# Optimization experiments

Hardware: AMD Instinct MI355X
Metric: run time of the kernel (lower is better)

The kernel has to match this reference:

```python
import jax, jax.numpy as jnp
import numpy as np

N_NODES = 100000
DIM = 256
N_SAMPLES = 64
N_CLASSES = 10


def setup_inputs() -> dict:
    key = jax.random.key(0)
    k1, k2, k3 = jax.random.split(key, 3)
    data = jax.random.normal(k1, (N_SAMPLES, DIM), dtype=jnp.float32)
    V = jax.random.uniform(k2, (N_NODES, DIM), dtype=jnp.float32)  # node matrix (torch.rand init)
    labels = jax.random.randint(k3, (N_SAMPLES,), 0, N_CLASSES)
    return {"data": data, "V": V, "labels": labels, "it": 0}


def reference(data, V, labels, it):
    # SOINN+ per-sample BMU search + BMU/sBMU weight pull, fixed node capacity.
    # eps schedules exactly as in ASOINN.forward.
    eps_b = 1.0 / (it + 2)
    eps_n = 1.0 / ((it + 1) * 100)

    def step(Vc, sample):
        # pairwise L2 distance of sample vs all nodes: [N]
        diff = sample[None, :] - Vc
        dists = jnp.sqrt(jnp.sum(diff * diff, axis=-1) + 1e-12)
        neg_vals, idx = jax.lax.top_k(-dists, 2)  # two smallest
        b, s = idx[0], idx[1]
        # update_bmu: V[b] += eps_b * (sample - V[b]); neighbor pull on sBMU
        Vc = Vc.at[b].add(eps_b * (sample - Vc[b]))
        Vc = Vc.at[s].add(eps_n * (sample - Vc[s]))
        return Vc, -neg_vals  # (b_dist, s_dist)

    V_final, bmu_dists = jax.lax.scan(step, V, data)
    return bmu_dists  # [N_SAMPLES, 2]
```

## Files before the change

kernel.cpp:

```cpp
#include <hip/hip_runtime.h>
#include <math.h>


#define N_NODES 100000
#define DIM     256
#define NS      64
#define NCH     1563
#define KC      32
#define NBMW    3125
#define CAP     4096
#define KL      192
#define KLS     136
#define NSP     10
#define NPW     8

typedef unsigned long long u64;

__device__ __forceinline__ u64 pk(float d, int i) {
  return ((u64)__float_as_uint(d) << 32) | (unsigned)i;
}
__device__ __forceinline__ u64 umin64(u64 a, u64 b) { return a < b ? a : b; }
__device__ __forceinline__ u64 umax64(u64 a, u64 b) { return a > b ? a : b; }
__device__ __forceinline__ void mrg2(u64& A0, u64& A1, u64 B0, u64 B1) {
  u64 m = umax64(A0, B0);
  A0 = umin64(A0, B0);
  A1 = umin64(umin64(A1, B1), m);
}

template <int C>
__device__ __forceinline__ u64 dpp64(u64 x) {
  unsigned lo = (unsigned)__builtin_amdgcn_update_dpp(
      (int)0xFFFFFFFF, (int)(unsigned)(x & 0xFFFFFFFFull), C, 0xF, 0xF, false);
  unsigned hi = (unsigned)__builtin_amdgcn_update_dpp(
      (int)0xFFFFFFFF, (int)(unsigned)(x >> 32), C, 0xF, 0xF, false);
  return ((u64)hi << 32) | lo;
}
template <int C>
__device__ __forceinline__ void dpp_round(u64& A0, u64& A1) {
  u64 B0 = dpp64<C>(A0);
  u64 B1 = dpp64<C>(A1);
  mrg2(A0, A1, B0, B1);
}

__global__ void k_xx(const float* __restrict__ X, float* __restrict__ XX) {
  int i = blockIdx.x, j = threadIdx.x;
  const float* xi = X + i * DIM;
  const float* xj = X + j * DIM;
  float acc = 0.f;
  for (int k = 0; k < DIM; k += 4) {
    float4 a = *(const float4*)(xi + k);
    float4 b = *(const float4*)(xj + k);
    acc += a.x * b.x + a.y * b.y + a.z * b.z + a.w * b.w;
  }
  XX[i * NS + j] = acc;
}

__global__ __launch_bounds__(256) void k_dist(const float* __restrict__ X,
                                              const float* __restrict__ V,
                                              const float* __restrict__ XX,
                                              float* __restrict__ P,
                                              float* __restrict__ PT,
                                              float* __restrict__ Q,
                                              u64* __restrict__ SUMC) {
  __shared__ float Xl[KC][68];
  __shared__ float Vl[KC][132];
  __shared__ float sq[128];
  const int tid = threadIdx.x;
  const int n0  = blockIdx.x * 128;
  const int ty  = tid >> 5;
  const int tx  = tid & 31;
  float acc[8][4];
#pragma unroll
  for (int i = 0; i < 8; i++)
#pragma unroll
    for (int u = 0; u < 4; u++) acc[i][u] = 0.f;
  float qa = 0.f;
  const int xsl = tid & 63;
  const int xkk = (tid >> 6) * 8;
  const int vn  = tid & 127;
  const int vkk = (tid >> 7) * 16;
  const bool vok = (n0 + vn < N_NODES);
  const float* vrow = V + (size_t)(n0 + vn) * DIM + vkk;
  const float* xrow = X + xsl * DIM + xkk;

  float4 xr0, xr1, vr[4];
  xr0 = *(const float4*)(xrow + 0);
  xr1 = *(const float4*)(xrow + 4);
#pragma unroll
  for (int m = 0; m < 4; m++)
    vr[m] = vok ? *(const float4*)(vrow + 4 * m) : make_float4(0.f, 0.f, 0.f, 0.f);

  for (int c = 0; c < 8; c++) {
    __syncthreads();
    Xl[xkk + 0][xsl] = xr0.x; Xl[xkk + 1][xsl] = xr0.y;
    Xl[xkk + 2][xsl] = xr0.z; Xl[xkk + 3][xsl] = xr0.w;
    Xl[xkk + 4][xsl] = xr1.x; Xl[xkk + 5][xsl] = xr1.y;
    Xl[xkk + 6][xsl] = xr1.z; Xl[xkk + 7][xsl] = xr1.w;
#pragma unroll
    for (int m = 0; m < 4; m++) {
      Vl[vkk + 4 * m + 0][vn] = vr[m].x; Vl[vkk + 4 * m + 1][vn] = vr[m].y;
      Vl[vkk + 4 * m + 2][vn] = vr[m].z; Vl[vkk + 4 * m + 3][vn] = vr[m].w;
    }
    __syncthreads();
    if (c + 1 < 8) {
      int kc = (c + 1) * KC;
      xr0 = *(const float4*)(xrow + kc);
      xr1 = *(const float4*)(xrow + kc + 4);
#pragma unroll
      for (int m = 0; m < 4; m++)
        vr[m] = vok ? *(const float4*)(vrow + kc + 4 * m)
                    : make_float4(0.f, 0.f, 0.f, 0.f);
    }
    if (tid < 128) {
      float qq = 0.f;
#pragma unroll 8
      for (int k = 0; k < KC; k++) { float t = Vl[k][tid]; qq += t * t; }
      qa += qq;
    }
#pragma unroll 4
    for (int k = 0; k < KC; k++) {
      float xs[8], vs[4];
      *(float4*)&xs[0] = *(const float4*)&Xl[k][ty * 8];
      *(float4*)&xs[4] = *(const float4*)&Xl[k][ty * 8 + 4];
      *(float4*)&vs[0] = *(const float4*)&Vl[k][tx * 4];
#pragma unroll
      for (int i = 0; i < 8; i++)
#pragma unroll
        for (int u = 0; u < 4; u++) acc[i][u] += xs[i] * vs[u];
    }
  }
  if (tid < 128) sq[tid] = qa;
  __syncthreads();
  if (tid < 128 && n0 + tid < N_NODES) Q[n0 + tid] = qa;
  float qs[4];
  *(float4*)&qs[0] = *(const float4*)&sq[tx * 4];
  const bool full = (n0 + 128) <= N_NODES;
#pragma unroll
  for (int i = 0; i < 8; i++) {
    int s = ty * 8 + i;
    float xn = XX[s * NS + s];
#pragma unroll
    for (int u = 0; u < 4; u++) acc[i][u] = xn - 2.f * acc[i][u] + qs[u];
    float* prow = P + (size_t)s * N_NODES + n0 + tx * 4;
    if (full) {
      *(float4*)(prow) = make_float4(acc[i][0], acc[i][1], acc[i][2], acc[i][3]);
    } else {
#pragma unroll
      for (int u = 0; u < 4; u++) {
        int n = n0 + tx * 4 + u;
        if (n < N_NODES) prow[u] = acc[i][u];
      }
    }
  }
#pragma unroll
  for (int u = 0; u < 4; u++) {
    int n = n0 + tx * 4 + u;
    if (n < N_NODES) {
      float* pt = PT + (size_t)n * NS + ty * 8;
      *(float4*)(pt)     = make_float4(acc[0][u], acc[1][u], acc[2][u], acc[3][u]);
      *(float4*)(pt + 4) = make_float4(acc[4][u], acc[5][u], acc[6][u], acc[7][u]);
    }
  }
#pragma unroll
  for (int i = 0; i < 8; i++) {
    int s = ty * 8 + i;
    u64 key = ~0ull;
#pragma unroll
    for (int u = 0; u < 4; u++) {
      int n = n0 + tx * 4 + u;
      if (n < N_NODES) key = umin64(key, pk(acc[i][u], n));
    }
#pragma unroll
    for (int off = 1; off <= 8; off <<= 1)
      key = umin64(key, (u64)__shfl_xor((unsigned long long)key, off, 64));
    if ((tx & 15) == 0) {
      int chunk = (n0 >> 6) + (tx >> 4);
      if (chunk < NCH) SUMC[(size_t)s * NCH + chunk] = key;
    }
  }
}

__global__ __launch_bounds__(1024) void k_build(const u64* __restrict__ SUMC,
                                                const float* __restrict__ P,
                                                u64* __restrict__ L) {
  __shared__ u64 A[CAP];
  __shared__ u64 Twave[16];
  __shared__ float Tsh;
  __shared__ int cnt;
  const int j = blockIdx.x, tid = threadIdx.x;
  const int w = tid >> 6, l = tid & 63;
  {
    int base = w * 98;
    u64 v0 = (base + l < NCH) ? SUMC[(size_t)j * NCH + base + l] : ~0ull;
    u64 v1 = (l < 34 && base + 64 + l < NCH)
                 ? SUMC[(size_t)j * NCH + base + 64 + l] : ~0ull;
    u64 s9 = ~0ull;
#pragma unroll
    for (int r = 0; r < 9; r++) {
      u64 m = umin64(v0, v1);
#pragma unroll
      for (int off = 1; off <= 32; off <<= 1)
        m = umin64(m, (u64)__shfl_xor((unsigned long long)m, off, 64));
      if (r == 8) { s9 = m; } else {
        if (v0 == m) v0 = ~0ull;
        if (v1 == m) v1 = ~0ull;
      }
    }
    if (l == 0) Twave[w] = s9;
  }
  __syncthreads();
  if (tid == 0) {
    u64 t = 0;
    for (int i = 0; i < 16; i++) t = umax64(t, Twave[i]);
    Tsh = __uint_as_float((unsigned)(t >> 32));
    cnt = 0;
  }
  __syncthreads();
  const float T = Tsh;
  const float* prow = P + (size_t)j * N_NODES;
  for (int n0 = tid * 4; n0 < N_NODES + 3; n0 += 4096) {
    float d[4];
    if (n0 + 3 < N_NODES) {
      float4 p = *(const float4*)(prow + n0);
      d[0] = p.x; d[1] = p.y; d[2] = p.z; d[3] = p.w;
    } else {
#pragma unroll
      for (int e = 0; e < 4; e++)
        d[e] = (n0 + e < N_NODES) ? prow[n0 + e] : INFINITY;
    }
#pragma unroll
    for (int e = 0; e < 4; e++) {
      if (d[e] <= T) {
        int pos = atomicAdd(&cnt, 1);
        if (pos < CAP) A[pos] = pk(d[e], n0 + e);
      }
    }
  }
  __syncthreads();
  int n = cnt; if (n > CAP) n = CAP;
  int M = 256; while (M < n) M <<= 1;
  for (int i = tid; i < M; i += 1024)
    if (i >= n) A[i] = ~0ull;
  __syncthreads();
  for (int k = 2; k <= M; k <<= 1)
    for (int s2 = k >> 1; s2 > 0; s2 >>= 1) {
      for (int i = tid; i < M; i += 1024) {
        int p = i ^ s2;
        if (p > i) {
          u64 a = A[i], b = A[p];
          bool up = ((i & k) == 0);
          if ((a > b) == up) { A[i] = b; A[p] = a; }
        }
      }
      __syncthreads();
    }
  for (int i = tid; i < KLS; i += 1024) L[(size_t)j * KL + i] = A[i];
}

__global__ __launch_bounds__(320) void k_seq(
    const float* __restrict__ PT, const float* __restrict__ Q,
    const float* __restrict__ XXg, const u64* __restrict__ L,
    const int* __restrict__ itp, float* __restrict__ out) {
  __shared__ float XXl[NS * 65];
  __shared__ float g[128][65];
  __shared__ float qv[128];
  __shared__ unsigned int bitmap[NBMW];
  __shared__ int tracked[128];
  __shared__ u64 cand16[NS][16];
  __shared__ float specg[8][NSP][NS];
  __shared__ float specq[8][NSP];
  __shared__ int   specid[8][NSP];
  __shared__ int ready[NS];
  __shared__ int done[NS];

  const int tid = threadIdx.x;
  const int wv = tid >> 6;
  const int lane = tid & 63;

  for (int i = tid; i < NS * NS; i += 320) {
    int r = i >> 6, c = i & 63;
    XXl[r * 65 + c] = XXg[i];
  }
  for (int i = tid; i < NBMW; i += 320) bitmap[i] = 0u;
  for (int i = tid; i < NS; i += 320) { ready[i] = 0; done[i] = 0; }
  __syncthreads();

  const int it = itp[0];
  const float eps_b = 1.0f / (float)(it + 2);
  const float eps_n = 1.0f / (float)((it + 1) * 100);
  const float xdl = XXl[lane * 65 + lane];

  if (wv == 0) {
    int ns = 0;
    int pw[NPW];
#pragma unroll
    for (int s = 0; s < NPW; s++) pw[s] = -1;
    for (int j = 0; j < NS; j++) {
      while (__hip_atomic_load(&ready[j], __ATOMIC_ACQUIRE,
                               __HIP_MEMORY_SCOPE_WORKGROUP) == 0)
        __builtin_amdgcn_s_sleep(1);
      const int sb = j & 7;
      u64 ck = (lane < 16) ? cand16[j][lane] : ~0ull;
      int sidl = (lane < NSP) ? specid[sb][lane] : -2;
      float gA = g[lane][j], gB = g[lane + 64][j];
      float qvA = qv[lane],  qvB = qv[lane + 64];
      int   tA = tracked[lane], tB = tracked[lane + 64];
      float xrow = XXl[j * 65 + lane];
      float xnj  = XXl[j * 65 + j];
      u64 A0 = ~0ull, A1 = ~0ull;
      {
        int id = (int)(unsigned)(ck & 0xFFFFFFFFull);
        bool ok = (ck != ~0ull);
#pragma unroll
        for (int s = 0; s < NPW; s++) ok = ok && (id != pw[s]);
        if (ok) { A0 = ck; }
      }
      if (lane < ns)      { float d = xnj - 2.f * gA + qvA; mrg2(A0, A1, pk(d, tA), ~0ull); }
      if (lane + 64 < ns) { float d = xnj - 2.f * gB + qvB; mrg2(A0, A1, pk(d, tB), ~0ull); }
      dpp_round<0x111>(A0, A1);
      dpp_round<0x112>(A0, A1);
      dpp_round<0x114>(A0, A1);
      dpp_round<0x118>(A0, A1);
      dpp_round<0x142>(A0, A1);
      dpp_round<0x143>(A0, A1);
      const int r0 = (int)(unsigned)__builtin_amdgcn_readlane(
          (int)(unsigned)(A0 & 0xFFFFFFFFull), 63);
      const int r1 = (int)(unsigned)__builtin_amdgcn_readlane(
          (int)(unsigned)(A1 & 0xFFFFFFFFull), 63);
      if (lane == 63) {
        float2 o;
        o.x = sqrtf(fmaxf(__uint_as_float((unsigned)(A0 >> 32)), 0.f) + 1e-12f);
        o.y = sqrtf(fmaxf(__uint_as_float((unsigned)(A1 >> 32)), 0.f) + 1e-12f);
        *(float2*)(out + j * 2) = o;
      }
      bool h0a = (lane < ns) && (tA == r0);
      bool h0b = (lane + 64 < ns) && (tB == r0);
      u64 mk0a = __ballot(h0a), mk0b = __ballot(h0b);
      bool new0 = (mk0a | mk0b) == 0ull;
      int sl0 = new0 ? ns
                     : (mk0a ? (__ffsll((unsigned long long)mk0a) - 1)
                             : (64 + __ffsll((unsigned long long)mk0b) - 1));
      bool h1a = (lane < ns) && (tA == r1);
      bool h1b = (lane + 64 < ns) && (tB == r1);
      u64 mk1a = __ballot(h1a), mk1b = __ballot(h1b);
      bool new1 = (mk1a | mk1b) == 0ull;
      int sl1 = new1 ? (ns + (new0 ? 1 : 0))
                     : (mk1a ? (__ffsll((unsigned long long)mk1a) - 1)
                             : (64 + __ffsll((unsigned long long)mk1b) - 1));
      u64 mh0 = __ballot(sidl == r0);
      u64 mh1 = __ballot(sidl == r1);
      bool hit0 = mh0 != 0ull, hit1 = mh1 != 0ull;
      int s0 = hit0 ? (__ffsll((unsigned long long)mh0) - 1) : 0;
      int s1 = hit1 ? (__ffsll((unsigned long long)mh1) - 1) : 0;
      float pv0 = specg[sb][s0][lane], qq0 = specq[sb][s0];
      float pv1 = specg[sb][s1][lane], qq1 = specq[sb][s1];
      if (new0 && !hit0) { pv0 = PT[(size_t)r0 * NS + lane]; qq0 = Q[r0]; }
      if (new1 && !hit1) { pv1 = PT[(size_t)r1 * NS + lane]; qq1 = Q[r1]; }
      float gt0 = g[sl0][lane];
      float gt1 = g[sl1][lane];
      float gold0 = new0 ? (0.5f * (xdl + qq0 - pv0)) : gt0;
      float qold0 = new0 ? qq0
                         : __uint_as_float((unsigned)__builtin_amdgcn_readlane(
                               (int)__float_as_uint(sl0 < 64 ? qvA : qvB), sl0 & 63));
      float gj0 = __uint_as_float(
          (unsigned)__builtin_amdgcn_readlane((int)__float_as_uint(gold0), j));
      g[sl0][lane] = (1.f - eps_b) * gold0 + eps_b * xrow;
      if (lane == 0) {
        float om = 1.f - eps_b;
        qv[sl0] = om * om * qold0 + 2.f * eps_b * om * gj0 + eps_b * eps_b * xnj;
        tracked[sl0] = r0;
        if (new0) bitmap[r0 >> 5] |= 1u << (r0 & 31);
      }
      float gold1 = new1 ? (0.5f * (xdl + qq1 - pv1)) : gt1;
      float qold1 = new1 ? qq1
                         : __uint_as_float((unsigned)__builtin_amdgcn_readlane(
                               (int)__float_as_uint(sl1 < 64 ? qvA : qvB), sl1 & 63));
      float gj1 = __uint_as_float(
          (unsigned)__builtin_amdgcn_readlane((int)__float_as_uint(gold1), j));
      g[sl1][lane] = (1.f - eps_n) * gold1 + eps_n * xrow;
      if (lane == 0) {
        float on = 1.f - eps_n;
        qv[sl1] = on * on * qold1 + 2.f * eps_n * on * gj1 + eps_n * eps_n * xnj;
        tracked[sl1] = r1;
        if (new1) bitmap[r1 >> 5] |= 1u << (r1 & 31);
      }
      ns += (new0 ? 1 : 0) + (new1 ? 1 : 0);
#pragma unroll
      for (int s = NPW - 1; s >= 2; s--) pw[s] = pw[s - 2];
      pw[0] = r0; pw[1] = r1;
      __hip_atomic_store(&done[j], 1, __ATOMIC_RELEASE,
                         __HIP_MEMORY_SCOPE_WORKGROUP);
    }
  } else {
    for (int t = wv - 1; t < NS; t += 4) {
      if (t >= 5) {
        while (__hip_atomic_load(&done[t - 5], __ATOMIC_ACQUIRE,
                                 __HIP_MEMORY_SCOPE_WORKGROUP) == 0)
          __builtin_amdgcn_s_sleep(1);
      }
      const u64* Lr = L + (size_t)t * KL;
      u64 e0 = Lr[lane], e1 = Lr[lane + 64];
      u64 e2 = (lane < 8) ? Lr[128 + lane] : ~0ull;
      int i0 = (int)(unsigned)(e0 & 0xFFFFFFFFull);
      int i1 = (int)(unsigned)(e1 & 0xFFFFFFFFull);
      int i2 = (int)(unsigned)(e2 & 0xFFFFFFFFull);
      bool t0 = (e0 == ~0ull) || ((bitmap[i0 >> 5] >> (i0 & 31)) & 1u);
      bool t1 = (e1 == ~0ull) || ((bitmap[i1 >> 5] >> (i1 & 31)) & 1u);
      bool t2 = (e2 == ~0ull) || ((bitmap[i2 >> 5] >> (i2 & 31)) & 1u);
      u64 um0 = ~__ballot(t0), um1 = ~__ballot(t1), um2 = ~__ballot(t2);
      u64 below = (1ull << lane) - 1;
      int c0n = __popcll((unsigned long long)um0);
      int c1n = __popcll((unsigned long long)um1);
      int rank0 = __popcll((unsigned long long)(um0 & below));
      int rank1 = c0n + __popcll((unsigned long long)(um1 & below));
      int rank2 = c0n + c1n + __popcll((unsigned long long)(um2 & below));
      if (!t0 && rank0 < 16) cand16[t][rank0] = e0;
      if (!t1 && rank1 < 16) cand16[t][rank1] = e1;
      if (!t2 && rank2 < 16) cand16[t][rank2] = e2;
      int U = c0n + c1n + __popcll((unsigned long long)um2);
      if (lane < 16 && lane >= U) cand16[t][lane] = ~0ull;
      const int sb = t & 7;
      int ids[NSP];
#pragma unroll
      for (int s = 0; s < NSP; s++)
        ids[s] = (int)(unsigned)(cand16[t][s] & 0xFFFFFFFFull);
#pragma unroll
      for (int s = 0; s < NSP; s++)
        specg[sb][s][lane] = PT[(size_t)ids[s] * NS + lane];
      if (lane < NSP) {
        specid[sb][lane] = ids[lane];
        specq[sb][lane] = Q[ids[lane]];
      }
      __hip_atomic_store(&ready[t], 1, __ATOMIC_RELEASE,
                         __HIP_MEMORY_SCOPE_WORKGROUP);
    }
  }
}

extern "C" void kernel_launch(void* const* d_in, const int* in_sizes, int n_in,
                              void* d_out, int out_size, void* d_ws, size_t ws_size,
                              hipStream_t stream) {
  const float* X  = (const float*)d_in[0];
  const float* V  = (const float*)d_in[1];
  const int*  itp = (const int*)d_in[3];
  float* out = (float*)d_out;

  char* ws = (char*)d_ws;
  size_t off = 0;
  auto alloc = [&](size_t bytes) -> void* {
    size_t o = (off + 255) & ~(size_t)255;
    off = o + bytes;
    return (void*)(ws + o);
  };
  float* P    = (float*)alloc((size_t)NS * N_NODES * sizeof(float));
  float* PT   = (float*)alloc((size_t)NS * N_NODES * sizeof(float));
  float* Q    = (float*)alloc((size_t)N_NODES * sizeof(float));
  float* XXp  = (float*)alloc((size_t)NS * NS * sizeof(float));
  u64*   SUMC = (u64*)alloc((size_t)NS * NCH * sizeof(u64));
  u64*   Lst  = (u64*)alloc((size_t)NS * KL * sizeof(u64));

  k_xx   <<<NS, NS, 0, stream>>>(X, XXp);
  k_dist <<<(N_NODES + 127) / 128, 256, 0, stream>>>(X, V, XXp, P, PT, Q, SUMC);
  k_build<<<NS, 1024, 0, stream>>>(SUMC, P, Lst);
  k_seq  <<<1, 320, 0, stream>>>(PT, Q, XXp, Lst, itp, out);
}
```

Before: 308.8 us.

## Pipeline next sample's candidate reduction into serial update loop of wave 0

The serial wave now computes the top-2 reduction for sample j+1 right after publishing the update for sample j. It excludes the two nodes just updated, and instead computes their fresh distances from the new g/q values and merges them in at the start of the next iteration. The intent is to shorten the critical dependency chain in the sequential BMU loop, so the DPP reduction no longer waits on the g/qv shared-memory writes. It adds register pressure and some subtle exclusion logic that must keep the same tie-breaking.

```diff
diff --git a/kernel.cpp b/kernel.cpp
--- a/kernel.cpp
+++ b/kernel.cpp
@@ -40,6 +40,17 @@
   u64 B0 = dpp64<C>(A0);
   u64 B1 = dpp64<C>(A1);
   mrg2(A0, A1, B0, B1);
+}
+__device__ __forceinline__ u64 rdl64(u64 x, int l) {
+  unsigned lo = (unsigned)__builtin_amdgcn_readlane(
+      (int)(unsigned)(x & 0xFFFFFFFFull), l);
+  unsigned hi = (unsigned)__builtin_amdgcn_readlane(
+      (int)(unsigned)(x >> 32), l);
+  return ((u64)hi << 32) | lo;
+}
+__device__ __forceinline__ float rdlf(float x, int l) {
+  return __uint_as_float(
+      (unsigned)__builtin_amdgcn_readlane((int)__float_as_uint(x), l));
 }
 
 __global__ void k_xx(const float* __restrict__ X, float* __restrict__ XX) {
@@ -295,44 +306,40 @@
     int pw[NPW];
 #pragma unroll
     for (int s = 0; s < NPW; s++) pw[s] = -1;
-    for (int j = 0; j < NS; j++) {
-      while (__hip_atomic_load(&ready[j], __ATOMIC_ACQUIRE,
+    u64 R0k, R1k;
+    {
+      while (__hip_atomic_load(&ready[0], __ATOMIC_ACQUIRE,
                                __HIP_MEMORY_SCOPE_WORKGROUP) == 0)
         __builtin_amdgcn_s_sleep(1);
-      const int sb = j & 7;
-      u64 ck = (lane < 16) ? cand16[j][lane] : ~0ull;
-      int sidl = (lane < NSP) ? specid[sb][lane] : -2;
-      float gA = g[lane][j], gB = g[lane + 64][j];
-      float qvA = qv[lane],  qvB = qv[lane + 64];
-      int   tA = tracked[lane], tB = tracked[lane + 64];
-      float xrow = XXl[j * 65 + lane];
-      float xnj  = XXl[j * 65 + j];
-      u64 A0 = ~0ull, A1 = ~0ull;
-      {
-        int id = (int)(unsigned)(ck & 0xFFFFFFFFull);
-        bool ok = (ck != ~0ull);
-#pragma unroll
-        for (int s = 0; s < NPW; s++) ok = ok && (id != pw[s]);
-        if (ok) { A0 = ck; }
-      }
-      if (lane < ns)      { float d = xnj - 2.f * gA + qvA; mrg2(A0, A1, pk(d, tA), ~0ull); }
-      if (lane + 64 < ns) { float d = xnj - 2.f * gB + qvB; mrg2(A0, A1, pk(d, tB), ~0ull); }
+      u64 A0 = (lane < 16) ? cand16[0][lane] : ~0ull;
+      u64 A1 = ~0ull;
       dpp_round<0x111>(A0, A1);
       dpp_round<0x112>(A0, A1);
       dpp_round<0x114>(A0, A1);
       dpp_round<0x118>(A0, A1);
       dpp_round<0x142>(A0, A1);
       dpp_round<0x143>(A0, A1);
-      const int r0 = (int)(unsigned)__builtin_amdgcn_readlane(
-          (int)(unsigned)(A0 & 0xFFFFFFFFull), 63);
-      const int r1 = (int)(unsigned)__builtin_amdgcn_readlane(
-          (int)(unsigned)(A1 & 0xFFFFFFFFull), 63);
-      if (lane == 63) {
+      R0k = rdl64(A0, 63); R1k = rdl64(A1, 63);
+    }
+    u64 fresh0k = ~0ull, fresh1k = ~0ull;
+
+    for (int j = 0; j < NS; j++) {
+      const int sb = j & 7;
+      u64 k0 = R0k, k1 = R1k;
+      mrg2(k0, k1, fresh0k, ~0ull);
+      mrg2(k0, k1, fresh1k, ~0ull);
+      const int r0 = (int)(unsigned)(k0 & 0xFFFFFFFFull);
+      const int r1 = (int)(unsigned)(k1 & 0xFFFFFFFFull);
+      if (lane == 0) {
         float2 o;
-        o.x = sqrtf(fmaxf(__uint_as_float((unsigned)(A0 >> 32)), 0.f) + 1e-12f);
-        o.y = sqrtf(fmaxf(__uint_as_float((unsigned)(A1 >> 32)), 0.f) + 1e-12f);
+        o.x = sqrtf(fmaxf(__uint_as_float((unsigned)(k0 >> 32)), 0.f) + 1e-12f);
+        o.y = sqrtf(fmaxf(__uint_as_float((unsigned)(k1 >> 32)), 0.f) + 1e-12f);
         *(float2*)(out + j * 2) = o;
       }
+      const float xnj = XXl[j * 65 + j];
+      const float xrow = XXl[j * 65 + lane];
+      int tA = tracked[lane], tB = tracked[lane + 64];
+      float qvA = qv[lane],  qvB = qv[lane + 64];
       bool h0a = (lane < ns) && (tA == r0);
       bool h0b = (lane + 64 < ns) && (tB == r0);
       u64 mk0a = __ballot(h0a), mk0b = __ballot(h0b);
@@ -347,6 +354,7 @@
       int sl1 = new1 ? (ns + (new0 ? 1 : 0))
                      : (mk1a ? (__ffsll((unsigned long long)mk1a) - 1)
                              : (64 + __ffsll((unsigned long long)mk1b) - 1));
+      int sidl = (lane < NSP) ? specid[sb][lane] : -2;
       u64 mh0 = __ballot(sidl == r0);
       u64 mh1 = __ballot(sidl == r1);
       bool hit0 = mh0 != 0ull, hit1 = mh1 != 0ull;
@@ -359,37 +367,68 @@
       float gt0 = g[sl0][lane];
       float gt1 = g[sl1][lane];
       float gold0 = new0 ? (0.5f * (xdl + qq0 - pv0)) : gt0;
-      float qold0 = new0 ? qq0
-                         : __uint_as_float((unsigned)__builtin_amdgcn_readlane(
-                               (int)__float_as_uint(sl0 < 64 ? qvA : qvB), sl0 & 63));
-      float gj0 = __uint_as_float(
-          (unsigned)__builtin_amdgcn_readlane((int)__float_as_uint(gold0), j));
-      g[sl0][lane] = (1.f - eps_b) * gold0 + eps_b * xrow;
+      float qold0 = new0 ? qq0 : rdlf(sl0 < 64 ? qvA : qvB, sl0 & 63);
+      float gj0 = rdlf(gold0, j);
+      float gnew0 = (1.f - eps_b) * gold0 + eps_b * xrow;
+      g[sl0][lane] = gnew0;
+      float om = 1.f - eps_b;
+      float qnew0 = om * om * qold0 + 2.f * eps_b * om * gj0 + eps_b * eps_b * xnj;
+      float gold1 = new1 ? (0.5f * (xdl + qq1 - pv1)) : gt1;
+      float qold1 = new1 ? qq1 : rdlf(sl1 < 64 ? qvA : qvB, sl1 & 63);
+      float gj1 = rdlf(gold1, j);
+      float gnew1 = (1.f - eps_n) * gold1 + eps_n * xrow;
+      g[sl1][lane] = gnew1;
+      float on = 1.f - eps_n;
+      float qnew1 = on * on * qold1 + 2.f * eps_n * on * gj1 + eps_n * eps_n * xnj;
       if (lane == 0) {
-        float om = 1.f - eps_b;
-        qv[sl0] = om * om * qold0 + 2.f * eps_b * om * gj0 + eps_b * eps_b * xnj;
+        qv[sl0] = qnew0;
         tracked[sl0] = r0;
         if (new0) bitmap[r0 >> 5] |= 1u << (r0 & 31);
-      }
-      float gold1 = new1 ? (0.5f * (xdl + qq1 - pv1)) : gt1;
-      float qold1 = new1 ? qq1
-                         : __uint_as_float((unsigned)__builtin_amdgcn_readlane(
-                               (int)__float_as_uint(sl1 < 64 ? qvA : qvB), sl1 & 63));
-      float gj1 = __uint_as_float(
-          (unsigned)__builtin_amdgcn_readlane((int)__float_as_uint(gold1), j));
-      g[sl1][lane] = (1.f - eps_n) * gold1 + eps_n * xrow;
-      if (lane == 0) {
-        float on = 1.f - eps_n;
-        qv[sl1] = on * on * qold1 + 2.f * eps_n * on * gj1 + eps_n * eps_n * xnj;
+        qv[sl1] = qnew1;
         tracked[sl1] = r1;
         if (new1) bitmap[r1 >> 5] |= 1u << (r1 & 31);
       }
+      const int nsb = ns;
       ns += (new0 ? 1 : 0) + (new1 ? 1 : 0);
 #pragma unroll
       for (int s = NPW - 1; s >= 2; s--) pw[s] = pw[s - 2];
       pw[0] = r0; pw[1] = r1;
       __hip_atomic_store(&done[j], 1, __ATOMIC_RELEASE,
                          __HIP_MEMORY_SCOPE_WORKGROUP);
+      if (j + 1 < NS) {
+        const float xn1 = XXl[(j + 1) * 65 + (j + 1)];
+        float d0 = xn1 - 2.f * rdlf(gnew0, j + 1) + qnew0;
+        fresh0k = pk(d0, r0);
+        float d1 = xn1 - 2.f * rdlf(gnew1, j + 1) + qnew1;
+        fresh1k = pk(d1, r1);
+        while (__hip_atomic_load(&ready[j + 1], __ATOMIC_ACQUIRE,
+                                 __HIP_MEMORY_SCOPE_WORKGROUP) == 0)
+          __builtin_amdgcn_s_sleep(1);
+        u64 ckn = (lane < 16) ? cand16[j + 1][lane] : ~0ull;
+        u64 A0 = ~0ull, A1 = ~0ull;
+        {
+          int id = (int)(unsigned)(ckn & 0xFFFFFFFFull);
+          bool ok = (ckn != ~0ull);
+#pragma unroll
+          for (int s = 0; s < NPW; s++) ok = ok && (id != pw[s]);
+          if (ok) A0 = ckn;
+        }
+        if (lane < nsb && tA != r0 && tA != r1) {
+          float d = xn1 - 2.f * g[lane][j + 1] + qvA;
+          mrg2(A0, A1, pk(d, tA), ~0ull);
+        }
+        if (lane + 64 < nsb && tB != r0 && tB != r1) {
+          float d = xn1 - 2.f * g[lane + 64][j + 1] + qvB;
+          mrg2(A0, A1, pk(d, tB), ~0ull);
+        }
+        dpp_round<0x111>(A0, A1);
+        dpp_round<0x112>(A0, A1);
+        dpp_round<0x114>(A0, A1);
+        dpp_round<0x118>(A0, A1);
+        dpp_round<0x142>(A0, A1);
+        dpp_round<0x143>(A0, A1);
+        R0k = rdl64(A0, 63); R1k = rdl64(A1, 63);
+      }
     }
   } else {
     for (int t = wv - 1; t < NS; t += 4) {
```

New measurement: 318.2 us. 1.03x slower.
